# Kernel optimization log

Hardware: AMD Instinct MI355X
Metric: run time of the kernel (lower is better)

Reference implementation:

```python
import jax, jax.numpy as jnp
import numpy as np
from jax import lax
import math

B, C_IN, C_OUT, D, H, W = 8, 32, 32, 16, 64, 64
K = 3            # kernel_size (cubic)
PAD = 1
E = 8            # num_experts
GROUPS = 1


def setup_inputs() -> dict:
    key = jax.random.key(0)
    k1, k2, k3, k4 = jax.random.split(key, 4)
    x = jax.random.normal(k1, (B, C_IN, D, H, W), dtype=jnp.float32)
    routing_weights = jax.random.uniform(k2, (B, E), dtype=jnp.float32)
    # kaiming_uniform_(a=sqrt(5)) equivalent bounds
    fan_in = (C_IN // GROUPS) * K * K * K
    gain = math.sqrt(2.0 / (1.0 + 5.0))
    w_bound = gain * math.sqrt(3.0 / fan_in)
    weight = jax.random.uniform(k3, (E, C_OUT, C_IN // GROUPS, K, K, K),
                                dtype=jnp.float32, minval=-w_bound, maxval=w_bound)
    b_bound = 1.0 / math.sqrt(fan_in)
    bias = jax.random.uniform(k4, (E, C_OUT), dtype=jnp.float32,
                              minval=-b_bound, maxval=b_bound)
    return {"x": x, "routing_weights": routing_weights, "weight": weight, "bias": bias}


def reference(x, routing_weights, weight, bias):
    # Faithful to the original einsum: 'bi,eocdwh->bocdwh' sums i and e
    # independently (outer-sum semantics), exactly as torch.einsum does.
    eff_kernel = jnp.einsum('bi,eocdwh->bocdwh', routing_weights, weight)  # [B,O,I/g,kd,kh,kw]
    eff_bias = jnp.einsum('bi,eo->bo', routing_weights, bias)              # [B,O]

    def conv_one(xi, ki, bi):
        # xi: [C_in,D,H,W]; ki: [O, I/g, kd,kh,kw]
        y = lax.conv_general_dilated(
            xi[None], ki,
            window_strides=(1, 1, 1),
            padding=[(PAD, PAD)] * 3,
            lhs_dilation=(1, 1, 1),
            rhs_dilation=(1, 1, 1),
            dimension_numbers=('NCDHW', 'OIDHW', 'NCDHW'),
            feature_group_count=GROUPS,
        )[0]
        return y + bi[:, None, None, None]

    return jax.vmap(conv_one)(x, eff_kernel, eff_bias)  # [B, C_OUT, D, H, W]
```

## Files before the change

### kernel.cpp

```cpp
#include <hip/hip_runtime.h>
#include <hip/hip_bf16.h>

typedef short short8 __attribute__((ext_vector_type(8)));
typedef short short4v __attribute__((ext_vector_type(4)));
typedef float f32x4 __attribute__((ext_vector_type(4)));

#define WF_OFF  0u
#define RWB_OFF 55296u
#define RWS_OFF 56320u

#define XS 72
#define RS (66 * XS)
#define PLANE (10 * RS)

__device__ __forceinline__ unsigned bf16rne(float f) {
    unsigned u = __float_as_uint(f);
    return (u + 0x7FFFu + ((u >> 16) & 1u)) >> 16;
}

__global__ void condconv_prep(const float* __restrict__ rw,
                              const float* __restrict__ weight,
                              const float* __restrict__ bias,
                              char* __restrict__ ws) {
    int i = blockIdx.x * 256 + threadIdx.x;
    if (i < 27648) {
        int t   = i >> 10;
        int rem = i & 1023;
        int ot  = rem >> 9;
        int l   = (rem >> 3) & 63;
        int j   = rem & 7;
        int o   = ot * 16 + (l & 15);
        int c   = 8 * (l >> 4) + j;
        float s = 0.f;
#pragma unroll
        for (int e = 0; e < 8; ++e) s += weight[((e * 32 + o) * 32 + c) * 27 + t];
        ((unsigned short*)(ws + WF_OFF))[i] = (unsigned short)bf16rne(s);
    } else if (i < 27904) {
        int k = i - 27648;
        int b = k >> 5, o = k & 31;
        float rs = 0.f, bs = 0.f;
#pragma unroll
        for (int e = 0; e < 8; ++e) { rs += rw[b * 8 + e]; bs += bias[e * 32 + o]; }
        ((float*)(ws + RWB_OFF))[k] = rs * bs;
        if (o == 0) ((float*)(ws + RWS_OFF))[b] = rs;
    }
}

__global__ __launch_bounds__(256, 3) void condconv_fused(
        const float* __restrict__ x,
        const char* __restrict__ wf,
        const float* __restrict__ rwbias,
        const float* __restrict__ rwsum,
        float* __restrict__ out) {
    __shared__ __align__(16) char smem[PLANE];

    const int tid  = threadIdx.x;
    const int wv   = tid >> 6;
    const int lane = tid & 63;
    const int n    = lane & 15;
    const int quad = lane >> 4;
    const int y0   = blockIdx.x * 8;
    const int z    = blockIdx.y;
    const int b    = blockIdx.z;
    const int xn   = wv * 16 + n;

    if (tid < 80) {
        int yp = tid >> 3, side = (tid >> 2) & 1, q = tid & 3;
        *(uint4*)(smem + yp * RS + side * (65 * XS) + q * 16) = make_uint4(0, 0, 0, 0);
    }

    f32x4 acc[2][8] = {};
    const float* xb = x + (size_t)b * 2097152;
    const char* wbase = wf + lane * 16;

#pragma unroll
    for (int dz = 0; dz < 3; ++dz) {
        const int gz = z + dz - 1;
        const bool gzok = (unsigned)gz < 16u;

        __syncthreads();
        if (gzok) {
#pragma unroll
            for (int it = 0; it < 5; ++it) {
                const int s  = it * 256 + tid;
                const int x4 = s & 15;
                const int c4 = (s >> 4) & 7;
                const int yp = s >> 7;
                const int gy = y0 + yp - 1;
                float4 v0 = {0, 0, 0, 0}, v1 = v0, v2 = v0, v3 = v0;
                if ((unsigned)gy < 64u) {
                    const float* p = xb + (size_t)c4 * 262144 + gz * 4096 + gy * 64 + 4 * x4;
                    v0 = *(const float4*)(p);
                    v1 = *(const float4*)(p + 65536);
                    v2 = *(const float4*)(p + 131072);
                    v3 = *(const float4*)(p + 196608);
                }
                const float a0[4] = {v0.x, v0.y, v0.z, v0.w};
                const float a1[4] = {v1.x, v1.y, v1.z, v1.w};
                const float a2[4] = {v2.x, v2.y, v2.z, v2.w};
                const float a3[4] = {v3.x, v3.y, v3.z, v3.w};
#pragma unroll
                for (int xi = 0; xi < 4; ++xi) {
                    union { __hip_bfloat162 h2[2]; uint2 u; } g;
                    g.h2[0] = __float22bfloat162_rn(make_float2(a0[xi], a1[xi]));
                    g.h2[1] = __float22bfloat162_rn(make_float2(a2[xi], a3[xi]));
                    const int X = 4 * x4 + xi + 1;
                    const int slot = c4 ^ ((X >> 2) & 7);
                    *(uint2*)(smem + yp * RS + X * XS + slot * 8) = g.u;
                }
            }
        }
        __syncthreads();

        if (gzok) {
            short8 wreg[18];
            const char* wp = wbase + dz * 18432;
#pragma unroll
            for (int t = 0; t < 18; ++t) wreg[t] = *(const short8*)(wp + t * 1024);
#pragma unroll
            for (int yq = 0; yq < 10; ++yq) {
#pragma unroll
                for (int dx = 0; dx < 3; ++dx) {
                    const int X = xn + dx;
                    const char* rowp = smem + yq * RS + X * XS;
                    const int s8 = (X >> 2) & 7;
                    union { short8 v; short4v h[2]; } xf;
                    xf.h[0] = *(const short4v*)(rowp + (((2 * quad + 0) ^ s8) << 3));
                    xf.h[1] = *(const short4v*)(rowp + (((2 * quad + 1) ^ s8) << 3));
#pragma unroll
                    for (int dy = 0; dy < 3; ++dy) {
                        const int r = yq - dy;
                        if (r >= 0 && r < 8) {
                            acc[0][r] = __builtin_amdgcn_mfma_f32_16x16x32_bf16(
                                wreg[(dy * 3 + dx) * 2 + 0], xf.v, acc[0][r], 0, 0, 0);
                            acc[1][r] = __builtin_amdgcn_mfma_f32_16x16x32_bf16(
                                wreg[(dy * 3 + dx) * 2 + 1], xf.v, acc[1][r], 0, 0, 0);
                        }
                    }
                }
            }
        }
    }

    const float rwb = rwsum[b];
#pragma unroll
    for (int ot = 0; ot < 2; ++ot)
#pragma unroll
        for (int reg = 0; reg < 4; ++reg) {
            const int o = ot * 16 + quad * 4 + reg;
            const float bb = rwbias[b * 32 + o];
            const size_t obase = ((size_t)(b * 32 + o) * 16 + z) * 64;
#pragma unroll
            for (int r = 0; r < 8; ++r)
                out[(obase + y0 + r) * 64 + xn] = rwb * acc[ot][r][reg] + bb;
        }
}

extern "C" void kernel_launch(void* const* d_in, const int* in_sizes, int n_in,
                              void* d_out, int out_size, void* d_ws, size_t ws_size,
                              hipStream_t stream) {
    const float* x      = (const float*)d_in[0];
    const float* rw     = (const float*)d_in[1];
    const float* weight = (const float*)d_in[2];
    const float* bias   = (const float*)d_in[3];
    float* out = (float*)d_out;
    char*  ws  = (char*)d_ws;

    condconv_prep<<<109, 256, 0, stream>>>(rw, weight, bias, ws);
    condconv_fused<<<dim3(8, 16, 8), 256, 0, stream>>>(
        x, ws + WF_OFF,
        (const float*)(ws + RWB_OFF), (const float*)(ws + RWS_OFF), out);
}
```

Before: 150.6 us.

## Prefetch next depth plane into registers during MFMA compute

Global loads for the next z-plane of input are issued into registers right after the LDS fill barrier, so they overlap the MFMA loop of the current plane. The converted bf16 data is written to shared memory at the start of the next iteration. This adds 80 float registers of prefetch state, so launch bounds are relaxed from 3 to 2 blocks per SIMD, which lowers occupancy and lets the compiler use more registers.

```diff
diff --git a/kernel.cpp b/kernel.cpp
--- a/kernel.cpp
+++ b/kernel.cpp
@@ -46,7 +46,7 @@
     }
 }
 
-__global__ __launch_bounds__(256, 3) void condconv_fused(
+__global__ __launch_bounds__(256, 2) void condconv_fused(
         const float* __restrict__ x,
         const char* __restrict__ wf,
         const float* __restrict__ rwbias,
@@ -73,6 +73,33 @@
     const float* xb = x + (size_t)b * 2097152;
     const char* wbase = wf + lane * 16;
 
+    float4 pv[5][4];
+
+    auto LOADP = [&](const int gz) {
+#pragma unroll
+        for (int it = 0; it < 5; ++it) {
+            const int s  = it * 256 + tid;
+            const int x4 = s & 15;
+            const int c4 = (s >> 4) & 7;
+            const int yp = s >> 7;
+            const int gy = y0 + yp - 1;
+            if ((unsigned)gy < 64u) {
+                const float* p = xb + (size_t)c4 * 262144 + gz * 4096 + gy * 64 + 4 * x4;
+                pv[it][0] = *(const float4*)(p);
+                pv[it][1] = *(const float4*)(p + 65536);
+                pv[it][2] = *(const float4*)(p + 131072);
+                pv[it][3] = *(const float4*)(p + 196608);
+            } else {
+                pv[it][0] = make_float4(0.f, 0.f, 0.f, 0.f);
+                pv[it][1] = make_float4(0.f, 0.f, 0.f, 0.f);
+                pv[it][2] = make_float4(0.f, 0.f, 0.f, 0.f);
+                pv[it][3] = make_float4(0.f, 0.f, 0.f, 0.f);
+            }
+        }
+    };
+
+    if (z > 0) LOADP(z - 1);
+
 #pragma unroll
     for (int dz = 0; dz < 3; ++dz) {
         const int gz = z + dz - 1;
@@ -86,19 +113,10 @@
                 const int x4 = s & 15;
                 const int c4 = (s >> 4) & 7;
                 const int yp = s >> 7;
-                const int gy = y0 + yp - 1;
-                float4 v0 = {0, 0, 0, 0}, v1 = v0, v2 = v0, v3 = v0;
-                if ((unsigned)gy < 64u) {
-                    const float* p = xb + (size_t)c4 * 262144 + gz * 4096 + gy * 64 + 4 * x4;
-                    v0 = *(const float4*)(p);
-                    v1 = *(const float4*)(p + 65536);
-                    v2 = *(const float4*)(p + 131072);
-                    v3 = *(const float4*)(p + 196608);
-                }
-                const float a0[4] = {v0.x, v0.y, v0.z, v0.w};
-                const float a1[4] = {v1.x, v1.y, v1.z, v1.w};
-                const float a2[4] = {v2.x, v2.y, v2.z, v2.w};
-                const float a3[4] = {v3.x, v3.y, v3.z, v3.w};
+                const float a0[4] = {pv[it][0].x, pv[it][0].y, pv[it][0].z, pv[it][0].w};
+                const float a1[4] = {pv[it][1].x, pv[it][1].y, pv[it][1].z, pv[it][1].w};
+                const float a2[4] = {pv[it][2].x, pv[it][2].y, pv[it][2].z, pv[it][2].w};
+                const float a3[4] = {pv[it][3].x, pv[it][3].y, pv[it][3].z, pv[it][3].w};
 #pragma unroll
                 for (int xi = 0; xi < 4; ++xi) {
                     union { __hip_bfloat162 h2[2]; uint2 u; } g;
@@ -111,6 +129,8 @@
             }
         }
         __syncthreads();
+
+        if (dz < 2 && (unsigned)(gz + 1) < 16u) LOADP(gz + 1);
 
         if (gzok) {
             short8 wreg[18];
```

Measured after the change: 141.3 us. -6.2%, faster.

## Pre-transform input to swizzled bf16 and stream tiles into LDS via direct loads

Applied to the files above, without the earlier changes.

Adds a separate pass that converts x once into a channel-last, XOR-swizzled bf16 buffer in workspace. The conv kernel then fills LDS with global_load_lds DMA copies, using a zero page for out-of-range rows, instead of loading fp32, converting and scattering on every halo reload. It also remaps block indices so neighbouring z-slices of a batch share the cache. This costs an extra kernel launch, a 32 MB workspace round trip, and a fallback path when the workspace is too small.

```diff
diff --git a/kernel.cpp b/kernel.cpp
--- a/kernel.cpp
+++ b/kernel.cpp
@@ -8,14 +8,20 @@
 #define WF_OFF  0u
 #define RWB_OFF 55296u
 #define RWS_OFF 56320u
-
-#define XS 72
-#define RS (66 * XS)
-#define PLANE (10 * RS)
+#define ZP_OFF  57344u
+#define XB_OFF  65536u
+#define XB_BYTES 33554432u
+
 
 __device__ __forceinline__ unsigned bf16rne(float f) {
     unsigned u = __float_as_uint(f);
     return (u + 0x7FFFu + ((u >> 16) & 1u)) >> 16;
+}
+
+__device__ __forceinline__ void llds16(const void* g, void* l) {
+    __builtin_amdgcn_global_load_lds(
+        (const __attribute__((address_space(1))) unsigned int*)g,
+        (__attribute__((address_space(3))) unsigned int*)l, 16, 0, 0);
 }
 
 __global__ void condconv_prep(const float* __restrict__ rw,
@@ -46,14 +52,144 @@
     }
 }
 
-__global__ __launch_bounds__(256, 3) void condconv_fused(
-        const float* __restrict__ x,
-        const char* __restrict__ wf,
-        const float* __restrict__ rwbias,
-        const float* __restrict__ rwsum,
+__global__ __launch_bounds__(256) void condconv_xform(
+        const float* __restrict__ x, char* __restrict__ ws) {
+    const int tid = threadIdx.x;
+    if (blockIdx.x == 0)
+        *(uint4*)(ws + ZP_OFF + tid * 16) = make_uint4(0, 0, 0, 0);
+
+    const int yo = blockIdx.x & 7;
+    const int z  = (blockIdx.x >> 3) & 15;
+    const int b  = blockIdx.x >> 7;
+    const float* xb = x + (size_t)b * 2097152;
+    char* xrow0 = ws + XB_OFF + ((size_t)(b * 16 + z) * 64 + yo * 8) * 4096;
+
+#pragma unroll
+    for (int it = 0; it < 4; ++it) {
+        const int s  = it * 256 + tid;
+        const int x4 = s & 15;
+        const int c4 = (s >> 4) & 7;
+        const int yr = s >> 7;
+        const int y  = yo * 8 + yr;
+        const float* p = xb + (size_t)c4 * 262144 + z * 4096 + y * 64 + 4 * x4;
+        float4 v0 = *(const float4*)(p);
+        float4 v1 = *(const float4*)(p + 65536);
+        float4 v2 = *(const float4*)(p + 131072);
+        float4 v3 = *(const float4*)(p + 196608);
+        const float a0[4] = {v0.x, v0.y, v0.z, v0.w};
+        const float a1[4] = {v1.x, v1.y, v1.z, v1.w};
+        const float a2[4] = {v2.x, v2.y, v2.z, v2.w};
+        const float a3[4] = {v3.x, v3.y, v3.z, v3.w};
+        char* rowp = xrow0 + (size_t)yr * 4096;
+        const int slot = c4 ^ (x4 & 7);
+#pragma unroll
+        for (int xi = 0; xi < 4; ++xi) {
+            union { __hip_bfloat162 h2[2]; uint2 u; } g;
+            g.h2[0] = __float22bfloat162_rn(make_float2(a0[xi], a1[xi]));
+            g.h2[1] = __float22bfloat162_rn(make_float2(a2[xi], a3[xi]));
+            *(uint2*)(rowp + (4 * x4 + xi) * 64 + slot * 8) = g.u;
+        }
+    }
+}
+
+__global__ __launch_bounds__(256, 3) void condconv_fused_dma(
+        const char* __restrict__ ws,
+        float* __restrict__ out) {
+    __shared__ __align__(16) char smem[40960];
+
+    const int tid  = threadIdx.x;
+    const int wv   = tid >> 6;
+    const int lane = tid & 63;
+    const int n    = lane & 15;
+    const int quad = lane >> 4;
+
+    const int logical = (blockIdx.x & 7) * 128 + (blockIdx.x >> 3);
+    const int z  = logical & 15;
+    const int y0 = ((logical >> 4) & 7) * 8;
+    const int b  = logical >> 7;
+    const int xn = wv * 16 + n;
+
+    f32x4 acc[2][8] = {};
+    const char* wbase = ws + WF_OFF + lane * 16;
+    const char* xb16  = ws + XB_OFF + (size_t)(b * 16) * 64 * 4096;
+    const char* zp    = ws + ZP_OFF;
+
+#pragma unroll
+    for (int dz = 0; dz < 3; ++dz) {
+        const int gz = z + dz - 1;
+        const bool gzok = (unsigned)gz < 16u;
+
+        __syncthreads();
+        if (gzok) {
+            const char* pb = xb16 + (size_t)gz * 64 * 4096;
+            const int lo = wv * 1024 + lane * 16;
+#pragma unroll
+            for (int yp = 0; yp < 10; ++yp) {
+                const int gy = y0 + yp - 1;
+                const char* src = ((unsigned)gy < 64u) ? (pb + (size_t)gy * 4096 + lo)
+                                                       : (zp + lo);
+                llds16(src, smem + yp * 4096 + wv * 1024);
+            }
+        }
+        __syncthreads();
+
+        if (gzok) {
+            short8 wreg[18];
+            const char* wp = wbase + dz * 18432;
+#pragma unroll
+            for (int t = 0; t < 18; ++t) wreg[t] = *(const short8*)(wp + t * 1024);
+#pragma unroll
+            for (int yq = 0; yq < 10; ++yq) {
+#pragma unroll
+                for (int dx = 0; dx < 3; ++dx) {
+                    const int X  = xn + dx - 1;
+                    const bool ok = (unsigned)X < 64u;
+                    const int Xc = ok ? X : 0;
+                    const char* rowp = smem + yq * 4096 + Xc * 64;
+                    const int s8 = (Xc >> 2) & 7;
+                    union { short8 v; short4v h[2]; } xf;
+                    xf.h[0] = *(const short4v*)(rowp + (((2 * quad + 0) ^ s8) << 3));
+                    xf.h[1] = *(const short4v*)(rowp + (((2 * quad + 1) ^ s8) << 3));
+                    if (!ok) { xf.h[0] = short4v{0, 0, 0, 0}; xf.h[1] = short4v{0, 0, 0, 0}; }
+#pragma unroll
+                    for (int dy = 0; dy < 3; ++dy) {
+                        const int r = yq - dy;
+                        if (r >= 0 && r < 8) {
+                            acc[0][r] = __builtin_amdgcn_mfma_f32_16x16x32_bf16(
+                                wreg[(dy * 3 + dx) * 2 + 0], xf.v, acc[0][r], 0, 0, 0);
+                            acc[1][r] = __builtin_amdgcn_mfma_f32_16x16x32_bf16(
+                                wreg[(dy * 3 + dx) * 2 + 1], xf.v, acc[1][r], 0, 0, 0);
+                        }
+                    }
+                }
+            }
+        }
+    }
+
+    const float rwb = ((const float*)(ws + RWS_OFF))[b];
+    const float* rwbias = (const float*)(ws + RWB_OFF);
+#pragma unroll
+    for (int ot = 0; ot < 2; ++ot)
+#pragma unroll
+        for (int reg = 0; reg < 4; ++reg) {
+            const int o = ot * 16 + quad * 4 + reg;
+            const float bb = rwbias[b * 32 + o];
+            const size_t obase = ((size_t)(b * 32 + o) * 16 + z) * 64;
+#pragma unroll
+            for (int r = 0; r < 8; ++r)
+                out[(obase + y0 + r) * 64 + xn] = rwb * acc[ot][r][reg] + bb;
+        }
+}
+
+#define XS 72
+#define RS (66 * XS)
+#define PLANE (10 * RS)
+
+__global__ __launch_bounds__(256, 3) void condconv_fused_v0(
+        const float* __restrict__ x, const char* __restrict__ wf,
+        const float* __restrict__ rwbias, const float* __restrict__ rwsum,
         float* __restrict__ out) {
     __shared__ __align__(16) char smem[PLANE];
-
     const int tid  = threadIdx.x;
     const int wv   = tid >> 6;
     const int lane = tid & 63;
@@ -77,7 +213,6 @@
     for (int dz = 0; dz < 3; ++dz) {
         const int gz = z + dz - 1;
         const bool gzok = (unsigned)gz < 16u;
-
         __syncthreads();
         if (gzok) {
 #pragma unroll
@@ -111,7 +246,6 @@
             }
         }
         __syncthreads();
-
         if (gzok) {
             short8 wreg[18];
             const char* wp = wbase + dz * 18432;
@@ -167,7 +301,13 @@
     char*  ws  = (char*)d_ws;
 
     condconv_prep<<<109, 256, 0, stream>>>(rw, weight, bias, ws);
-    condconv_fused<<<dim3(8, 16, 8), 256, 0, stream>>>(
-        x, ws + WF_OFF,
-        (const float*)(ws + RWB_OFF), (const float*)(ws + RWS_OFF), out);
-}
+
+    if (ws_size >= (size_t)XB_OFF + XB_BYTES) {
+        condconv_xform<<<1024, 256, 0, stream>>>(x, ws);
+        condconv_fused_dma<<<1024, 256, 0, stream>>>(ws, out);
+    } else {
+        condconv_fused_v0<<<dim3(8, 16, 8), 256, 0, stream>>>(
+            x, ws + WF_OFF,
+            (const float*)(ws + RWB_OFF), (const float*)(ws + RWS_OFF), out);
+    }
+}
```

After: 169.7 us. 12.6% more time.

## Walk depth with a three-plane ring buffer and keep all weights in registers

Applied to the files above, without the earlier changes.

Replaces the per-output-plane kernel, which restaged three input planes per block, with a kernel that walks 8 consecutive z planes using a rotating 3-plane shared-memory ring. Each plane is staged once and reused across three outputs. The tiles become 8x16 in y/x, and each wave holds all 27 tap weights for one 16-channel output half in registers. The grid is remapped to 512 blocks and launch bounds drop to 2 blocks per CU, so each block now runs a longer serial loop with two barriers per z step and higher register pressure.

```diff
diff --git a/kernel.cpp b/kernel.cpp
--- a/kernel.cpp
+++ b/kernel.cpp
@@ -9,9 +9,10 @@
 #define RWB_OFF 55296u
 #define RWS_OFF 56320u
 
-#define XS 72
-#define RS (66 * XS)
-#define PLANE (10 * RS)
+#define XSB 72
+#define ROWB (24 * XSB)
+#define PLANE_B (10 * ROWB)
+#define RING_B (3 * PLANE_B)
 
 __device__ __forceinline__ unsigned bf16rne(float f) {
     unsigned u = __float_as_uint(f);
@@ -46,114 +47,140 @@
     }
 }
 
-__global__ __launch_bounds__(256, 3) void condconv_fused(
+__global__ __launch_bounds__(256, 2) void condconv_zwalk(
         const float* __restrict__ x,
         const char* __restrict__ wf,
         const float* __restrict__ rwbias,
         const float* __restrict__ rwsum,
         float* __restrict__ out) {
-    __shared__ __align__(16) char smem[PLANE];
+    __shared__ __align__(16) char smem[RING_B];
 
     const int tid  = threadIdx.x;
     const int wv   = tid >> 6;
     const int lane = tid & 63;
     const int n    = lane & 15;
     const int quad = lane >> 4;
-    const int y0   = blockIdx.x * 8;
-    const int z    = blockIdx.y;
-    const int b    = blockIdx.z;
-    const int xn   = wv * 16 + n;
-
-    if (tid < 80) {
-        int yp = tid >> 3, side = (tid >> 2) & 1, q = tid & 3;
-        *(uint4*)(smem + yp * RS + side * (65 * XS) + q * 16) = make_uint4(0, 0, 0, 0);
+    const int ot   = wv & 1;
+    const int yh   = wv >> 1;
+
+    const int logical = (blockIdx.x & 7) * 64 + (blockIdx.x >> 3);
+    const int b   = logical >> 6;
+    const int rem = logical & 63;
+    const int zb  = rem & 1;
+    const int xb  = (rem >> 1) & 3;
+    const int yb  = rem >> 3;
+    const int y0 = yb * 8, x0 = xb * 16, zr0 = zb * 8;
+
+    const float* xbp = x + (size_t)b * 2097152;
+
+    const bool sact = tid < 240;
+    const int  sx4  = tid % 6;
+    const int  syp  = (tid / 6) % 10;
+    const int  sc4h = tid / 60;
+    const int  gxq  = xb * 4 + sx4 - 1;
+    const int  gy   = y0 + syp - 1;
+    const bool gok  = ((unsigned)gxq < 16u) && ((unsigned)gy < 64u);
+    const long soff = (long)sc4h * 262144 + (long)(gok ? gy : 0) * 64 +
+                      (long)(gok ? gxq : 0) * 4;
+    const int woffA = syp * ROWB + (4 * sx4) * XSB + ((sc4h ^ sx4) << 3);
+    const int woffB = syp * ROWB + (4 * sx4) * XSB + (((sc4h + 4) ^ sx4) << 3);
+
+    short8 wreg[27];
+    {
+        const char* wb_ = wf + lane * 16 + ot * 1024;
+#pragma unroll
+        for (int t = 0; t < 27; ++t) wreg[t] = *(const short8*)(wb_ + t * 2048);
     }
 
-    f32x4 acc[2][8] = {};
-    const float* xb = x + (size_t)b * 2097152;
-    const char* wbase = wf + lane * 16;
-
-#pragma unroll
-    for (int dz = 0; dz < 3; ++dz) {
-        const int gz = z + dz - 1;
-        const bool gzok = (unsigned)gz < 16u;
-
+    const float rwb = rwsum[b];
+    float bb[4];
+#pragma unroll
+    for (int j = 0; j < 4; ++j) bb[j] = rwbias[b * 32 + ot * 16 + quad * 4 + j];
+    float* outb = out + (size_t)(b * 32 + ot * 16 + quad * 4) * 65536 +
+                  (size_t)(y0 + yh * 4) * 64 + x0 + n;
+
+    auto STAGE = [&](int p, char* pl) {
+        if (!sact) return;
+        float4 vA0 = {0,0,0,0}, vA1 = vA0, vA2 = vA0, vA3 = vA0;
+        float4 vB0 = vA0, vB1 = vA0, vB2 = vA0, vB3 = vA0;
+        if (gok && (unsigned)p < 16u) {
+            const float* q0 = xbp + soff + (long)p * 4096;
+            vA0 = *(const float4*)(q0);
+            vA1 = *(const float4*)(q0 + 65536);
+            vA2 = *(const float4*)(q0 + 131072);
+            vA3 = *(const float4*)(q0 + 196608);
+            const float* q1 = q0 + 1048576;
+            vB0 = *(const float4*)(q1);
+            vB1 = *(const float4*)(q1 + 65536);
+            vB2 = *(const float4*)(q1 + 131072);
+            vB3 = *(const float4*)(q1 + 196608);
+        }
+        const float A0[4] = {vA0.x, vA0.y, vA0.z, vA0.w};
+        const float A1[4] = {vA1.x, vA1.y, vA1.z, vA1.w};
+        const float A2[4] = {vA2.x, vA2.y, vA2.z, vA2.w};
+        const float A3[4] = {vA3.x, vA3.y, vA3.z, vA3.w};
+        const float B0[4] = {vB0.x, vB0.y, vB0.z, vB0.w};
+        const float B1[4] = {vB1.x, vB1.y, vB1.z, vB1.w};
+        const float B2[4] = {vB2.x, vB2.y, vB2.z, vB2.w};
+        const float B3[4] = {vB3.x, vB3.y, vB3.z, vB3.w};
+#pragma unroll
+        for (int xi = 0; xi < 4; ++xi) {
+            union { __hip_bfloat162 h2[2]; uint2 u; } gA, gB;
+            gA.h2[0] = __float22bfloat162_rn(make_float2(A0[xi], A1[xi]));
+            gA.h2[1] = __float22bfloat162_rn(make_float2(A2[xi], A3[xi]));
+            gB.h2[0] = __float22bfloat162_rn(make_float2(B0[xi], B1[xi]));
+            gB.h2[1] = __float22bfloat162_rn(make_float2(B2[xi], B3[xi]));
+            *(uint2*)(pl + woffA + xi * XSB) = gA.u;
+            *(uint2*)(pl + woffB + xi * XSB) = gB.u;
+        }
+    };
+
+    STAGE(zr0 - 1, smem + ((zr0 + 2) % 3) * PLANE_B);
+    STAGE(zr0,     smem + (zr0 % 3) * PLANE_B);
+
+    f32x4 acc[4] = {};
+
+    for (int zi = zr0; zi < zr0 + 8; ++zi) {
         __syncthreads();
-        if (gzok) {
-#pragma unroll
-            for (int it = 0; it < 5; ++it) {
-                const int s  = it * 256 + tid;
-                const int x4 = s & 15;
-                const int c4 = (s >> 4) & 7;
-                const int yp = s >> 7;
-                const int gy = y0 + yp - 1;
-                float4 v0 = {0, 0, 0, 0}, v1 = v0, v2 = v0, v3 = v0;
-                if ((unsigned)gy < 64u) {
-                    const float* p = xb + (size_t)c4 * 262144 + gz * 4096 + gy * 64 + 4 * x4;
-                    v0 = *(const float4*)(p);
-                    v1 = *(const float4*)(p + 65536);
-                    v2 = *(const float4*)(p + 131072);
-                    v3 = *(const float4*)(p + 196608);
-                }
-                const float a0[4] = {v0.x, v0.y, v0.z, v0.w};
-                const float a1[4] = {v1.x, v1.y, v1.z, v1.w};
-                const float a2[4] = {v2.x, v2.y, v2.z, v2.w};
-                const float a3[4] = {v3.x, v3.y, v3.z, v3.w};
-#pragma unroll
-                for (int xi = 0; xi < 4; ++xi) {
-                    union { __hip_bfloat162 h2[2]; uint2 u; } g;
-                    g.h2[0] = __float22bfloat162_rn(make_float2(a0[xi], a1[xi]));
-                    g.h2[1] = __float22bfloat162_rn(make_float2(a2[xi], a3[xi]));
-                    const int X = 4 * x4 + xi + 1;
-                    const int slot = c4 ^ ((X >> 2) & 7);
-                    *(uint2*)(smem + yp * RS + X * XS + slot * 8) = g.u;
-                }
-            }
-        }
+        STAGE(zi + 1, smem + ((zi + 1) % 3) * PLANE_B);
         __syncthreads();
 
-        if (gzok) {
-            short8 wreg[18];
-            const char* wp = wbase + dz * 18432;
-#pragma unroll
-            for (int t = 0; t < 18; ++t) wreg[t] = *(const short8*)(wp + t * 1024);
-#pragma unroll
-            for (int yq = 0; yq < 10; ++yq) {
+        const char* P[3] = { smem + ((zi + 2) % 3) * PLANE_B,
+                             smem + ((zi    ) % 3) * PLANE_B,
+                             smem + ((zi + 1) % 3) * PLANE_B };
+#pragma unroll
+        for (int dz = 0; dz < 3; ++dz) {
+#pragma unroll
+            for (int q = 0; q < 6; ++q) {
+                const char* rowq = P[dz] + (yh * 4 + q) * ROWB;
 #pragma unroll
                 for (int dx = 0; dx < 3; ++dx) {
-                    const int X = xn + dx;
-                    const char* rowp = smem + yq * RS + X * XS;
-                    const int s8 = (X >> 2) & 7;
+                    const int lx = n + dx + 3;
+                    const int s8 = lx >> 2;
+                    const char* rowp = rowq + lx * XSB;
                     union { short8 v; short4v h[2]; } xf;
                     xf.h[0] = *(const short4v*)(rowp + (((2 * quad + 0) ^ s8) << 3));
                     xf.h[1] = *(const short4v*)(rowp + (((2 * quad + 1) ^ s8) << 3));
 #pragma unroll
                     for (int dy = 0; dy < 3; ++dy) {
-                        const int r = yq - dy;
-                        if (r >= 0 && r < 8) {
-                            acc[0][r] = __builtin_amdgcn_mfma_f32_16x16x32_bf16(
-                                wreg[(dy * 3 + dx) * 2 + 0], xf.v, acc[0][r], 0, 0, 0);
-                            acc[1][r] = __builtin_amdgcn_mfma_f32_16x16x32_bf16(
-                                wreg[(dy * 3 + dx) * 2 + 1], xf.v, acc[1][r], 0, 0, 0);
-                        }
+                        const int r = q - dy;
+                        if (r >= 0 && r < 4)
+                            acc[r] = __builtin_amdgcn_mfma_f32_16x16x32_bf16(
+                                wreg[dz * 9 + dy * 3 + dx], xf.v, acc[r], 0, 0, 0);
                     }
                 }
             }
         }
+
+#pragma unroll
+        for (int r = 0; r < 4; ++r) {
+#pragma unroll
+            for (int j = 0; j < 4; ++j)
+                outb[(size_t)j * 65536 + (size_t)zi * 4096 + r * 64] =
+                    rwb * acc[r][j] + bb[j];
+            acc[r] = f32x4{0, 0, 0, 0};
+        }
     }
-
-    const float rwb = rwsum[b];
-#pragma unroll
-    for (int ot = 0; ot < 2; ++ot)
-#pragma unroll
-        for (int reg = 0; reg < 4; ++reg) {
-            const int o = ot * 16 + quad * 4 + reg;
-            const float bb = rwbias[b * 32 + o];
-            const size_t obase = ((size_t)(b * 32 + o) * 16 + z) * 64;
-#pragma unroll
-            for (int r = 0; r < 8; ++r)
-                out[(obase + y0 + r) * 64 + xn] = rwb * acc[ot][r][reg] + bb;
-        }
 }
 
 extern "C" void kernel_launch(void* const* d_in, const int* in_sizes, int n_in,
@@ -167,7 +194,7 @@
     char*  ws  = (char*)d_ws;
 
     condconv_prep<<<109, 256, 0, stream>>>(rw, weight, bias, ws);
-    condconv_fused<<<dim3(8, 16, 8), 256, 0, stream>>>(
+    condconv_zwalk<<<512, 256, 0, stream>>>(
         x, ws + WF_OFF,
         (const float*)(ws + RWB_OFF), (const float*)(ws + RWS_OFF), out);
 }
```

After: 148.9 us. Within noise of the previous version (-1.1%).
